# Optimization experiments

Measured on AMD Instinct MI355X. Metric: run time of the kernel, lower is better.

The kernel has to match this reference:

```python
import jax, jax.numpy as jnp
import numpy as np

B, S, T, E, H = 64, 256, 128, 256, 512


def setup_inputs() -> dict:
    key = jax.random.key(0)
    ks = jax.random.split(key, 12)
    sc = 0.05
    return {
        "trg_embed": jax.random.normal(ks[0], (B, T + 1, E), jnp.float32),
        "encoder_hidden": jax.random.normal(ks[1], (B, S, 2 * H), jnp.float32),
        "encoder_final": jax.random.normal(ks[2], (B, H), jnp.float32),
        "src_mask": jnp.ones((B, S), bool),
        "W_ih": jax.random.normal(ks[3], (3 * H, E + 2 * H), jnp.float32) * sc,
        "W_hh": jax.random.normal(ks[4], (3 * H, H), jnp.float32) * sc,
        "b_ih": jnp.zeros((3 * H,), jnp.float32),
        "b_hh": jnp.zeros((3 * H,), jnp.float32),
        "bridge_w": jax.random.normal(ks[5], (H, H), jnp.float32) * sc,
        "bridge_b": jnp.zeros((H,), jnp.float32),
        "key_w": jax.random.normal(ks[6], (H, 2 * H), jnp.float32) * sc,
        "query_w": jax.random.normal(ks[7], (H, H), jnp.float32) * sc,
        "energy_w": jax.random.normal(ks[8], (H,), jnp.float32) * sc,
        "pre_w": jax.random.normal(ks[9], (2 * H, H + 2 * H + E), jnp.float32) * sc,
        "pre_b": jnp.zeros((2 * H,), jnp.float32),
        "max_len": T,
    }


def reference(trg_embed, encoder_hidden, encoder_final, src_mask,
              W_ih, W_hh, b_ih, b_hh, bridge_w, bridge_b,
              key_w, query_w, energy_w, pre_w, pre_b, max_len):
    # bridge: initial decoder state from final encoder state
    h0 = jnp.tanh(encoder_final @ bridge_w.T + bridge_b)          # [B,H]
    # precomputed attention keys
    proj_key = jnp.einsum('bsk,hk->bsh', encoder_hidden, key_w)   # [B,S,H]
    neg = jnp.asarray(-1e9, trg_embed.dtype)

    prev = jnp.swapaxes(trg_embed[:, :max_len], 0, 1)             # [T,B,E]
    curr = jnp.swapaxes(trg_embed[:, 1:max_len + 1], 0, 1)        # [T,B,E] (generate_first)

    def step(h, pc):
        p, c = pc
        # --- additive (Bahdanau) attention, query = current hidden ---
        q = h @ query_w.T                                         # [B,H]
        scores = jnp.tanh(q[:, None, :] + proj_key) @ energy_w    # [B,S]
        scores = jnp.where(src_mask, scores, neg)
        alphas = jax.nn.softmax(scores, axis=-1)                  # [B,S]
        context = jnp.einsum('bs,bsd->bd', alphas, encoder_hidden)  # [B,2H]
        # --- generate_first: pre_output from previous hidden ---
        pre_out = jnp.concatenate([p, h, context], axis=-1) @ pre_w.T + pre_b  # [B,2H]
        # --- GRU cell (torch gate order r, z, n) ---
        x = jnp.concatenate([c, context], axis=-1)                # [B,E+2H]
        gi = x @ W_ih.T + b_ih
        gh = h @ W_hh.T + b_hh
        ir, iz, inn = jnp.split(gi, 3, axis=-1)
        hr, hz, hn = jnp.split(gh, 3, axis=-1)
        r = jax.nn.sigmoid(ir + hr)
        z = jax.nn.sigmoid(iz + hz)
        n = jnp.tanh(inn + r * hn)
        h_new = (1 - z) * n + z * h
        return h_new, (h_new, pre_out, alphas)

    h_fin, (states, pre_outs, attns) = jax.lax.scan(step, h0, (prev, curr))
    return (jnp.swapaxes(states, 0, 1),      # [B,T,H] decoder_states
            h_fin,                            # [B,H] final hidden
            jnp.swapaxes(pre_outs, 0, 1),     # [B,T,2H] pre_output_vectors
            jnp.swapaxes(attns, 0, 1))        # [B,T,S] attention_vectors
```

## Files before the change

### kernel.cpp

```cpp
#include <hip/hip_runtime.h>
#include <hip/hip_fp16.h>

using u32 = unsigned int;

constexpr int B = 64, S = 256, T = 128, E = 256, H = 512, H2 = 1024;
constexpr int TE = (T + 1) * E;

constexpr size_t OUT_HFIN = (size_t)B * T * H;
constexpr size_t OUT_PRE  = OUT_HFIN + (size_t)B * H;
constexpr size_t OUT_ATT  = OUT_PRE + (size_t)B * T * H2;

constexpr size_t WS_HPREV = 0;
constexpr size_t WS_QWT4  = 32768;
constexpr size_t WS_TRGT  = WS_QWT4 + 131072;
constexpr size_t WS_PK2   = WS_TRGT + 1056768;
constexpr size_t WS_HT2R  = WS_PK2 + 4194304;
constexpr size_t WS_QBUF  = WS_HT2R + (size_t)129 * 16384;
constexpr size_t WS_CTXR  = WS_QBUF + (size_t)128 * 16384;
constexpr size_t WS_SEWR  = WS_CTXR + (size_t)128 * 32768;
constexpr size_t WS_BAR   = WS_SEWR + 65536;
constexpr size_t WS_WFR   = WS_BAR + 2048;
constexpr size_t WS_TOTAL = WS_WFR + (size_t)192 * 3584 * 4;

constexpr int L_EHS = 0;
constexpr int L_EWP = 65536;
constexpr int L_HP  = 66688;
constexpr int L_SH2 = 67200;
constexpr int L_UNI = 68224;
constexpr int L_QRED = L_UNI;
constexpr int L_SSE  = L_UNI;
constexpr int L_CRC  = L_UNI;
constexpr int L_SST  = L_UNI + 6144;
constexpr int SMEM_BYTES = L_UNI + 8192;

typedef _Float16 half8 __attribute__((ext_vector_type(8)));
typedef float    f32x4 __attribute__((ext_vector_type(4)));
union UH  { u32 u; _Float16 h[2]; };
union UH8 { uint4 v; half8 h; };

__device__ __forceinline__ u32 pkh(float a, float b) {
  auto v = __builtin_amdgcn_cvt_pkrtz(a, b);
  u32 r; __builtin_memcpy(&r, &v, 4); return r;
}
__device__ __forceinline__ float f16lo(u32 u) { UH x; x.u = u; return (float)x.h[0]; }
__device__ __forceinline__ float f16hi(u32 u) { UH x; x.u = u; return (float)x.h[1]; }

#if __has_builtin(__builtin_amdgcn_fdot2)
__device__ __forceinline__ float fdot2(u32 a, u32 b, float c) {
  typedef _Float16 h2t __attribute__((ext_vector_type(2)));
  h2t av, bv; __builtin_memcpy(&av, &a, 4); __builtin_memcpy(&bv, &b, 4);
  return __builtin_amdgcn_fdot2(av, bv, c, false);
}
#else
__device__ __forceinline__ float fdot2(u32 a, u32 b, float c) {
  return c + f16lo(a) * f16lo(b) + f16hi(a) * f16hi(b);
}
#endif

__device__ __forceinline__ float fast_tanh(float x) {
  return 1.0f - 2.0f / (__expf(2.0f * x) + 1.0f);
}
__device__ __forceinline__ float fast_sigmoid(float x) {
  return 1.0f / (1.0f + __expf(-x));
}
__device__ __forceinline__ float dot4(float4 a, float4 b) {
  return a.x * b.x + a.y * b.y + a.z * b.z + a.w * b.w;
}

__device__ __forceinline__ void st_wt(u32* p, u32 v) {
  __hip_atomic_store(p, v, __ATOMIC_RELAXED, __HIP_MEMORY_SCOPE_AGENT);
}
__device__ __forceinline__ void st_wt_f(float* p, float v) {
  union { float f; u32 u; } c; c.f = v;
  __hip_atomic_store((u32*)p, c.u, __ATOMIC_RELAXED, __HIP_MEMORY_SCOPE_AGENT);
}

__device__ __forceinline__ void gbar_arrive(u32* barg, int p, u32 n) {
  asm volatile("s_waitcnt vmcnt(0) lgkmcnt(0)" ::: "memory");
  __syncthreads();
  if (threadIdx.x == 0) {
    u32 old = __hip_atomic_fetch_add(barg + (p >> 4) * 32, 1u,
                                     __ATOMIC_RELAXED, __HIP_MEMORY_SCOPE_AGENT);
    if ((old & 15u) == 15u) {
      u32 r = __hip_atomic_fetch_add(barg + 768, 1u,
                                     __ATOMIC_RELAXED, __HIP_MEMORY_SCOPE_AGENT);
      if ((r & 15u) == 15u)
        __hip_atomic_store(barg + 800, n, __ATOMIC_RELAXED, __HIP_MEMORY_SCOPE_AGENT);
    }
  }
}
__device__ __forceinline__ void gbar_wait(u32* barg, u32 n) {
  if (threadIdx.x == 0) {
    while (__hip_atomic_load(barg + 800, __ATOMIC_RELAXED,
                             __HIP_MEMORY_SCOPE_AGENT) < n)
      __builtin_amdgcn_s_sleep(2);
  }
  __syncthreads();
  asm volatile("" ::: "memory");
}

__global__ void bridge_kernel(const float* __restrict__ ef,
                              const float* __restrict__ bw,
                              const float* __restrict__ bb,
                              float* __restrict__ h0T) {
  int gid = blockIdx.x * blockDim.x + threadIdx.x;
  int j = gid >> 6, b = gid & 63;
  const float4* w = (const float4*)(bw + (size_t)j * H);
  const float4* e = (const float4*)(ef + (size_t)b * H);
  float acc = 0.f;
#pragma unroll 4
  for (int k = 0; k < H / 4; ++k) acc += dot4(w[k], e[k]);
  h0T[gid] = tanhf(acc + bb[j]);
}

__global__ void packh0_kernel(const float* __restrict__ hprevT, u32* __restrict__ hT2) {
  int idx = blockIdx.x * 512 + threadIdx.x;
  int dp = idx >> 6, b = idx & 63;
  hT2[(size_t)(dp >> 2) * 256 + b * 4 + (dp & 3)] =
      pkh(hprevT[(size_t)(2 * dp) * 64 + b], hprevT[(size_t)(2 * dp + 1) * 64 + b]);
}

__global__ void qwt4_kernel(const float* __restrict__ qw, uint4* __restrict__ qwt4) {
  int kq = blockIdx.x, j = threadIdx.x;
  const float* src = qw + (size_t)j * H + kq * 8;
  uint4 o;
  o.x = pkh(src[0], src[1]); o.y = pkh(src[2], src[3]);
  o.z = pkh(src[4], src[5]); o.w = pkh(src[6], src[7]);
  qwt4[(size_t)kq * 512 + j] = o;
}

__global__ void trgT2_kernel(const float* __restrict__ trg, u32* __restrict__ trgT) {
  int b = blockIdx.x, tid = threadIdx.x;
  for (int i = 0; i < 33; ++i) {
    int idx = i * 512 + tid;
    if (idx >= 129 * 128) break;
    int tt = idx >> 7, kp = idx & 127;
    float2 v = *(const float2*)(trg + (size_t)b * TE + (size_t)tt * 256 + kp * 2);
    trgT[(size_t)tt * 8192 + (size_t)(kp >> 2) * 256 + b * 4 + (kp & 3)] = pkh(v.x, v.y);
  }
}

__global__ void wfrag_kernel(const float* __restrict__ W_ih,
                             const float* __restrict__ W_hh,
                             const float* __restrict__ pre_w,
                             uint4* __restrict__ wfr) {
  const int p = blockIdx.x;
  const bool isGate = p < 128;
  for (int idx = threadIdx.x; idx < 56 * 64; idx += 512) {
    int ks = idx >> 6, lane = idx & 63;
    u32 w4[4];
#pragma unroll
    for (int i = 0; i < 4; ++i) {
      int kp = ks * 16 + (lane >> 4) * 4 + i;
      float a = 0.f, bv = 0.f;
      if (isGate) {
        int row = lane & 15, jo = row >> 2, g = row & 3;
        int j = p * 4 + jo;
        if (kp < 128) {
          if (g < 3) { const float* s_ = W_ih + (size_t)(g * 512 + j) * 1280 + kp * 2; a = s_[0]; bv = s_[1]; }
        } else if (kp < 384) {
          int c = (kp - 128) * 2;
          if (g < 2)       { const float* s_ = W_hh + (size_t)(g * 512 + j) * 512 + c; a = s_[0]; bv = s_[1]; }
          else if (g == 3) { const float* s_ = W_hh + (size_t)(1024 + j) * 512 + c;    a = s_[0]; bv = s_[1]; }
        } else {
          if (g < 3) { const float* s_ = W_ih + (size_t)(g * 512 + j) * 1280 + 256 + (kp - 384) * 2; a = s_[0]; bv = s_[1]; }
        }
      } else {
        int row = (p - 128) * 16 + (lane & 15);
        int c = (kp < 128) ? kp * 2 : (kp < 384) ? 256 + (kp - 128) * 2 : 768 + (kp - 384) * 2;
        const float* s_ = pre_w + (size_t)row * 1792 + c;
        a = s_[0]; bv = s_[1];
      }
      w4[i] = pkh(a, bv);
    }
    wfr[(size_t)p * 3584 + idx] = make_uint4(w4[0], w4[1], w4[2], w4[3]);
  }
}

__global__ void __launch_bounds__(256, 4) projkey2_kernel(
    const float* __restrict__ eh, const float* __restrict__ key_w,
    u32* __restrict__ pk) {
  constexpr int ST = 68;
  __shared__ float ea[64][ST];
  __shared__ float kb[64][ST];
  const int b  = blockIdx.x;
  const int s0 = blockIdx.y * 64;
  const int j0 = blockIdx.z * 64;
  const int tid = threadIdx.x;
  const int rl = tid >> 2, ql = tid & 3;
  const int tx = tid & 15, ty = tid >> 4;
  float acc[4][4] = {};
  const float* esrc = eh + ((size_t)b * S + s0 + rl) * H2;
  const float* ksrc = key_w + (size_t)(j0 + rl) * H2;
  for (int kc = 0; kc < H2; kc += 64) {
    float4 ev[4], kv[4];
#pragma unroll
    for (int m = 0; m < 4; ++m) {
      ev[m] = *(const float4*)(esrc + kc + ql * 16 + m * 4);
      kv[m] = *(const float4*)(ksrc + kc + ql * 16 + m * 4);
    }
    __syncthreads();
#pragma unroll
    for (int m = 0; m < 4; ++m) {
#pragma unroll
      for (int c = 0; c < 4; ++c) {
        int k = ql * 16 + m * 4 + c;
        ea[k][rl] = (&ev[m].x)[c];
        kb[k][rl] = (&kv[m].x)[c];
      }
    }
    __syncthreads();
#pragma unroll 8
    for (int k = 0; k < 64; ++k) {
      float4 a4 = *(const float4*)&ea[k][ty * 4];
      float4 b4 = *(const float4*)&kb[k][tx * 4];
      float av[4] = {a4.x, a4.y, a4.z, a4.w};
      float bv[4] = {b4.x, b4.y, b4.z, b4.w};
#pragma unroll
      for (int i = 0; i < 4; ++i)
#pragma unroll
        for (int jj = 0; jj < 4; ++jj) acc[i][jj] += av[i] * bv[jj];
    }
  }
#pragma unroll
  for (int i = 0; i < 4; ++i) {
    int s = s0 + ty * 4 + i;
    u32 u0 = pkh(acc[i][0], acc[i][1]);
    u32 u1 = pkh(acc[i][2], acc[i][3]);
    *(uint2*)(pk + (size_t)(b * S + s) * 256 + j0 / 2 + tx * 2) = make_uint2(u0, u1);
  }
}

__global__ void __launch_bounds__(512, 4) decoder_loop(
    const float* __restrict__ eh,
    const float* __restrict__ b_ih, const float* __restrict__ b_hh,
    const float* __restrict__ energy_w, const float* __restrict__ pre_b,
    float* __restrict__ out, float* __restrict__ ws) {
  __builtin_amdgcn_fence(__ATOMIC_ACQUIRE, "agent");

  extern __shared__ char smem[];
  u32*   ehs  = (u32*)(smem + L_EHS);
  u32*   ewp  = (u32*)(smem + L_EWP);
  float* shp  = (float*)(smem + L_HP);
  u32*   sh2  = (u32*)(smem + L_SH2);
  float* qred = (float*)(smem + L_QRED);
  float* sse  = (float*)(smem + L_SSE);
  float* crc  = (float*)(smem + L_CRC);
  float* sst  = (float*)(smem + L_SST);

  const uint4* qwt4 = (const uint4*)(ws + WS_QWT4);
  const u32* trgT = (const u32*)(ws + WS_TRGT);
  const u32* pk2  = (const u32*)(ws + WS_PK2);
  const uint4* wfru = (const uint4*)(ws + WS_WFR);
  u32*   ht2r = (u32*)(ws + WS_HT2R);
  u32*   qbr  = (u32*)(ws + WS_QBUF);
  u32*   ctxr = (u32*)(ws + WS_CTXR);
  float* sewr = ws + WS_SEWR;

  const int P = blockIdx.x, tid = threadIdx.x;
  const int g = P >> 8, p = P & 255;
  u32* barg = (u32*)(ws + WS_BAR) + (size_t)g * 1024;
  const int lane = tid & 63, wid = tid >> 6;
  const int b_loc = p >> 3, slice8 = p & 7, s0 = slice8 * 32;
  const int b = g * 32 + b_loc;
  const int bt = wid & 1, kseg = wid >> 1;
  const int bcol = bt * 16 + (lane & 15);
  const int gb = g * 32 + bcol;
  const int g4 = lane >> 4;
  const bool isG = p < 192, isGate = p < 128;

  for (int idx = tid; idx < 32 * 512; idx += 512) {
    int s = idx >> 9, dp = idx & 511;
    float2 v = *(const float2*)(eh + (size_t)(b * 256 + s0 + s) * 1024 + 2 * dp);
    ehs[idx] = pkh(v.x, v.y);
  }
  if (tid < 256)
    ewp[(tid >> 4) * 17 + (tid & 15)] = pkh(energy_w[tid * 2], energy_w[tid * 2 + 1]);
  if (isGate && tid < 128) {
    int jo = tid >> 5, b2 = tid & 31;
    shp[tid] = ws[WS_HPREV + (size_t)(p * 4 + jo) * 64 + (g * 32 + b2)];
  }
  __syncthreads();

  u32 bid = 0;
  for (int t = 0; t < T; ++t) {
    u32* ht2c = ht2r + (size_t)t * 16384;
    u32* ht2n = ht2r + (size_t)(t + 1) * 16384;
    u32* qbt  = qbr + (size_t)t * 16384;
    u32* ctxt = ctxr + (size_t)t * 32768;

    if (tid < 256)
      sh2[tid] = ht2c[(size_t)(tid >> 2) * 256 + b * 4 + (tid & 3)];
    __syncthreads();
    {
      const int jj = slice8 * 64 + lane;
      float acc = 0.f;
#pragma unroll
      for (int kk = 0; kk < 8; ++kk) {
        int kq = wid * 8 + kk;
        uint4 w = qwt4[(size_t)kq * 512 + jj];
        acc = fdot2(w.x, sh2[kq * 4 + 0], acc);
        acc = fdot2(w.y, sh2[kq * 4 + 1], acc);
        acc = fdot2(w.z, sh2[kq * 4 + 2], acc);
        acc = fdot2(w.w, sh2[kq * 4 + 3], acc);
      }
      qred[lane * 9 + wid] = acc;
    }
    __syncthreads();
    if (tid < 32) {
      float q0 = 0.f, q1 = 0.f;
#pragma unroll
      for (int i = 0; i < 8; ++i) { q0 += qred[(2 * tid) * 9 + i]; q1 += qred[(2 * tid + 1) * 9 + i]; }
      st_wt(qbt + (size_t)b * 256 + slice8 * 32 + tid, pkh(q0, q1));
    }
    gbar_arrive(barg, p, ++bid);
    uint4 pk4[4];
    {
      const uint4* pq = (const uint4*)(pk2 + (size_t)(b * 256 + s0 + (tid >> 4)) * 256) + (tid & 15) * 4;
#pragma unroll
      for (int i = 0; i < 4; ++i) pk4[i] = pq[i];
    }
    gbar_wait(barg, bid);

    {
      const int s = tid >> 4, jo = tid & 15;
      const uint4* qrow = (const uint4*)(qbt + (size_t)b * 256) + jo * 4;
      float acc = 0.f;
#pragma unroll
      for (int i = 0; i < 4; ++i) {
        uint4 q4 = qrow[i];
        uint4 pv = pk4[i];
#pragma unroll
        for (int c = 0; c < 4; ++c) {
          u32 qw = (&q4.x)[c];
          u32 w = (&pv.x)[c];
          u32 ew = ewp[jo * 17 + i * 4 + c];
          acc += fast_tanh(f16lo(qw) + f16lo(w)) * f16lo(ew) +
                 fast_tanh(f16hi(qw) + f16hi(w)) * f16hi(ew);
        }
      }
      acc += __shfl_xor(acc, 1); acc += __shfl_xor(acc, 2);
      acc += __shfl_xor(acc, 4); acc += __shfl_xor(acc, 8);
      if ((lane & 15) == 0) {
        float e = __expf(acc);
        out[OUT_ATT + ((size_t)b * T + t) * 256 + s0 + s] = e;
        sse[s] = e;
      }
    }
    __syncthreads();
    if (tid < 32) {
      float sv = sse[tid];
      for (int d = 16; d; d >>= 1) sv += __shfl_xor(sv, d);
      if (tid == 0) st_wt_f(sewr + (size_t)t * 512 + g * 256 + p, sv);
    }
    {
      float a0 = 0.f, a1 = 0.f;
      const u32* er = ehs + tid;
#pragma unroll 8
      for (int s2 = 0; s2 < 32; ++s2) {
        u32 uu = er[s2 * 512];
        float es = sse[s2];
        a0 += es * f16lo(uu);
        a1 += es * f16hi(uu);
      }
      __half2 v2 = __floats2half2_rn(a0, a1);
      unsafeAtomicAdd((__half2*)(ctxt + (size_t)(tid >> 2) * 256 + b * 4 + (tid & 3)), v2);
    }
    gbar_arrive(barg, p, ++bid);
    f32x4 ceh = {0.f, 0.f, 0.f, 0.f}, cct = {0.f, 0.f, 0.f, 0.f};
    if (isG) {
      const u32* embB = trgT + (size_t)(isGate ? t + 1 : t) * 8192;
#pragma unroll
      for (int i = 0; i < 6; ++i) {
        int ks = kseg + 4 * i;
        const u32* bsrc = (ks < 8) ? embB : ht2c;
        int kq = (ks < 8) ? ks : ks - 8;
        UH8 a_, b_;
        a_.v = wfru[((size_t)p * 56 + ks) * 64 + lane];
        b_.v = *(const uint4*)(bsrc + (size_t)((kq * 4 + g4) * 256 + gb * 4));
        ceh = __builtin_amdgcn_mfma_f32_16x16x32_f16(a_.h, b_.h, ceh, 0, 0, 0);
      }
    }
    gbar_wait(barg, bid);

    if (isG) {
#pragma unroll
      for (int i = 6; i < 14; ++i) {
        int ks = kseg + 4 * i;
        UH8 a_, b_;
        a_.v = wfru[((size_t)p * 56 + ks) * 64 + lane];
        b_.v = *(const uint4*)(ctxt + (size_t)(((ks - 24) * 4 + g4) * 256 + gb * 4));
        cct = __builtin_amdgcn_mfma_f32_16x16x32_f16(a_.h, b_.h, cct, 0, 0, 0);
      }
      const float* sp = sewr + (size_t)t * 512 + g * 256 + bcol * 8;
      float4 sv0 = *(const float4*)sp;
      float4 sv1 = *(const float4*)(sp + 4);
      float rv = 1.f / (sv0.x + sv0.y + sv0.z + sv0.w + sv1.x + sv1.y + sv1.z + sv1.w);
      f32x4 tot;
#pragma unroll
      for (int r = 0; r < 4; ++r) tot[r] = ceh[r] + rv * cct[r];
      if (kseg != 0) {
        float* cc = crc + (size_t)((bt * 3 + kseg - 1) * 64 + lane) * 4;
        cc[0] = tot[0]; cc[1] = tot[1]; cc[2] = tot[2]; cc[3] = tot[3];
      }
      __syncthreads();
      if (kseg == 0) {
#pragma unroll
        for (int i = 0; i < 3; ++i) {
          const float* cc = crc + (size_t)((bt * 3 + i) * 64 + lane) * 4;
          tot[0] += cc[0]; tot[1] += cc[1]; tot[2] += cc[2]; tot[3] += cc[3];
        }
        if (isGate) {
          int j = p * 4 + g4;
          float r = fast_sigmoid(tot[0] + b_ih[j] + b_hh[j]);
          float z = fast_sigmoid(tot[1] + b_ih[512 + j] + b_hh[512 + j]);
          float n = fast_tanh((tot[2] + b_ih[1024 + j]) + r * (tot[3] + b_hh[1024 + j]));
          float hp = shp[g4 * 32 + bcol];
          float hv = (1.f - z) * n + z * hp;
          shp[g4 * 32 + bcol] = hv;
          float ho = __shfl_xor(hv, 16);
          if ((g4 & 1) == 0) {
            int jp = p * 2 + (g4 >> 1);
            st_wt(ht2n + (size_t)(jp >> 2) * 256 + gb * 4 + (jp & 3), pkh(hv, ho));
          }
          sst[g4 * 32 + bcol] = hv;
        } else {
          int prow = (p - 128) * 16 + g4 * 4;
          sst[(g4 * 4 + 0) * 32 + bcol] = tot[0] + pre_b[prow + 0];
          sst[(g4 * 4 + 1) * 32 + bcol] = tot[1] + pre_b[prow + 1];
          sst[(g4 * 4 + 2) * 32 + bcol] = tot[2] + pre_b[prow + 2];
          sst[(g4 * 4 + 3) * 32 + bcol] = tot[3] + pre_b[prow + 3];
        }
      }
      __syncthreads();
      if (isGate) {
        if (tid < 32) {
          int b2 = g * 32 + tid;
          float4 o = make_float4(sst[0 * 32 + tid], sst[1 * 32 + tid],
                                 sst[2 * 32 + tid], sst[3 * 32 + tid]);
          *(float4*)(out + ((size_t)b2 * T + t) * 512 + p * 4) = o;
          if (t == T - 1)
            *(float4*)(out + OUT_HFIN + (size_t)b2 * 512 + p * 4) = o;
        }
      } else {
        if (tid < 128) {
          int b2 = g * 32 + (tid & 31), q4 = tid >> 5;
          float4 o = make_float4(sst[(q4 * 4 + 0) * 32 + (tid & 31)],
                                 sst[(q4 * 4 + 1) * 32 + (tid & 31)],
                                 sst[(q4 * 4 + 2) * 32 + (tid & 31)],
                                 sst[(q4 * 4 + 3) * 32 + (tid & 31)]);
          *(float4*)(out + OUT_PRE + ((size_t)b2 * T + t) * 1024 + (p - 128) * 16 + q4 * 4) = o;
        }
      }
    }
    gbar_arrive(barg, p, ++bid);
    if (tid < 32) {
      const float* sp = sewr + (size_t)t * 512 + g * 256 + b_loc * 8;
      float4 sv0 = *(const float4*)sp;
      float4 sv1 = *(const float4*)(sp + 4);
      float rinv = 1.f / (sv0.x + sv0.y + sv0.z + sv0.w + sv1.x + sv1.y + sv1.z + sv1.w);
      out[OUT_ATT + ((size_t)b * T + t) * 256 + s0 + tid] *= rinv;
    }
    if (t == T - 1) break;
    gbar_wait(barg, bid);
  }
}

extern "C" void kernel_launch(void* const* d_in, const int* in_sizes, int n_in,
                              void* d_out, int out_size, void* d_ws, size_t ws_size,
                              hipStream_t stream) {
  const float* trg      = (const float*)d_in[0];
  const float* eh       = (const float*)d_in[1];
  const float* ef       = (const float*)d_in[2];
  const float* W_ih     = (const float*)d_in[4];
  const float* W_hh     = (const float*)d_in[5];
  const float* b_ih     = (const float*)d_in[6];
  const float* b_hh     = (const float*)d_in[7];
  const float* bridge_w = (const float*)d_in[8];
  const float* bridge_b = (const float*)d_in[9];
  const float* key_w    = (const float*)d_in[10];
  const float* query_w  = (const float*)d_in[11];
  const float* energy_w = (const float*)d_in[12];
  const float* pre_w    = (const float*)d_in[13];
  const float* pre_b    = (const float*)d_in[14];
  float* out = (float*)d_out;
  float* ws  = (float*)d_ws;

  hipMemsetAsync((char*)d_ws + WS_CTXR * sizeof(float), 0,
                 (WS_WFR - WS_CTXR) * sizeof(float), stream);
  bridge_kernel<<<64, 512, 0, stream>>>(ef, bridge_w, bridge_b, ws + WS_HPREV);
  packh0_kernel<<<32, 512, 0, stream>>>(ws + WS_HPREV, (u32*)(ws + WS_HT2R));
  qwt4_kernel<<<64, 512, 0, stream>>>(query_w, (uint4*)(ws + WS_QWT4));
  trgT2_kernel<<<64, 512, 0, stream>>>(trg, (u32*)(ws + WS_TRGT));
  wfrag_kernel<<<192, 512, 0, stream>>>(W_ih, W_hh, pre_w, (uint4*)(ws + WS_WFR));
  projkey2_kernel<<<dim3(B, S / 64, H / 64), 256, 0, stream>>>(eh, key_w,
                                                               (u32*)(ws + WS_PK2));

  hipFuncSetAttribute((const void*)decoder_loop,
                      hipFuncAttributeMaxDynamicSharedMemorySize, SMEM_BYTES);
  decoder_loop<<<dim3(512), dim3(512), SMEM_BYTES, stream>>>(
      eh, b_ih, b_hh, energy_w, pre_b, out, ws);
}
```

Measured before the change: 3.580 ms.

## Replace group-wide barrier after query with per-batch 8-block barrier; hoist proj_key loads

The barrier after writing the query vector involved all 256 blocks in a group. It is replaced with a local counter barrier over only the 8 blocks that share a batch row, since only they consume that row's query. The proj_key slice is also loaded once into registers before the time loop rather than reloaded every step. This trades 16 extra VGPRs and a second barrier counter region for fewer global synchronisation round-trips per timestep.

```diff
diff --git a/kernel.cpp b/kernel.cpp
--- a/kernel.cpp
+++ b/kernel.cpp
@@ -19,7 +19,7 @@
 constexpr size_t WS_CTXR  = WS_QBUF + (size_t)128 * 16384;
 constexpr size_t WS_SEWR  = WS_CTXR + (size_t)128 * 32768;
 constexpr size_t WS_BAR   = WS_SEWR + 65536;
-constexpr size_t WS_WFR   = WS_BAR + 2048;
+constexpr size_t WS_WFR   = WS_BAR + 4096;
 constexpr size_t WS_TOTAL = WS_WFR + (size_t)192 * 3584 * 4;
 
 constexpr int L_EHS = 0;
@@ -94,6 +94,18 @@
     while (__hip_atomic_load(barg + 800, __ATOMIC_RELAXED,
                              __HIP_MEMORY_SCOPE_AGENT) < n)
       __builtin_amdgcn_s_sleep(2);
+  }
+  __syncthreads();
+  asm volatile("" ::: "memory");
+}
+
+__device__ __forceinline__ void bbar(u32* cnt, u32 target) {
+  asm volatile("s_waitcnt vmcnt(0) lgkmcnt(0)" ::: "memory");
+  __syncthreads();
+  if (threadIdx.x == 0) {
+    __hip_atomic_fetch_add(cnt, 1u, __ATOMIC_RELAXED, __HIP_MEMORY_SCOPE_AGENT);
+    while (__hip_atomic_load(cnt, __ATOMIC_RELAXED, __HIP_MEMORY_SCOPE_AGENT) < target)
+      __builtin_amdgcn_s_sleep(1);
   }
   __syncthreads();
   asm volatile("" ::: "memory");
@@ -263,6 +275,7 @@
   const int lane = tid & 63, wid = tid >> 6;
   const int b_loc = p >> 3, slice8 = p & 7, s0 = slice8 * 32;
   const int b = g * 32 + b_loc;
+  u32* barb = (u32*)(ws + WS_BAR) + 2048 + (size_t)(g * 32 + b_loc) * 32;
   const int bt = wid & 1, kseg = wid >> 1;
   const int bcol = bt * 16 + (lane & 15);
   const int gb = g * 32 + bcol;
@@ -280,9 +293,17 @@
     int jo = tid >> 5, b2 = tid & 31;
     shp[tid] = ws[WS_HPREV + (size_t)(p * 4 + jo) * 64 + (g * 32 + b2)];
   }
+  u32 pkr[16];
+  {
+    const u32* pq = pk2 + (size_t)(b * 256 + s0 + (tid >> 4)) * 256 + (tid & 15) * 16;
+#pragma unroll
+    for (int i = 0; i < 16; ++i) pkr[i] = pq[i];
+#pragma unroll
+    for (int i = 0; i < 16; ++i) asm volatile("" : "+v"(pkr[i]));
+  }
   __syncthreads();
 
-  u32 bid = 0;
+  u32 gbid = 0;
   for (int t = 0; t < T; ++t) {
     u32* ht2c = ht2r + (size_t)t * 16384;
     u32* ht2n = ht2r + (size_t)(t + 1) * 16384;
@@ -313,14 +334,7 @@
       for (int i = 0; i < 8; ++i) { q0 += qred[(2 * tid) * 9 + i]; q1 += qred[(2 * tid + 1) * 9 + i]; }
       st_wt(qbt + (size_t)b * 256 + slice8 * 32 + tid, pkh(q0, q1));
     }
-    gbar_arrive(barg, p, ++bid);
-    uint4 pk4[4];
-    {
-      const uint4* pq = (const uint4*)(pk2 + (size_t)(b * 256 + s0 + (tid >> 4)) * 256) + (tid & 15) * 4;
-#pragma unroll
-      for (int i = 0; i < 4; ++i) pk4[i] = pq[i];
-    }
-    gbar_wait(barg, bid);
+    bbar(barb, 8u * (u32)(t + 1));
 
     {
       const int s = tid >> 4, jo = tid & 15;
@@ -329,11 +343,10 @@
 #pragma unroll
       for (int i = 0; i < 4; ++i) {
         uint4 q4 = qrow[i];
-        uint4 pv = pk4[i];
 #pragma unroll
         for (int c = 0; c < 4; ++c) {
           u32 qw = (&q4.x)[c];
-          u32 w = (&pv.x)[c];
+          u32 w = pkr[i * 4 + c];
           u32 ew = ewp[jo * 17 + i * 4 + c];
           acc += fast_tanh(f16lo(qw) + f16lo(w)) * f16lo(ew) +
                  fast_tanh(f16hi(qw) + f16hi(w)) * f16hi(ew);
@@ -366,7 +379,7 @@
       __half2 v2 = __floats2half2_rn(a0, a1);
       unsafeAtomicAdd((__half2*)(ctxt + (size_t)(tid >> 2) * 256 + b * 4 + (tid & 3)), v2);
     }
-    gbar_arrive(barg, p, ++bid);
+    gbar_arrive(barg, p, ++gbid);
     f32x4 ceh = {0.f, 0.f, 0.f, 0.f}, cct = {0.f, 0.f, 0.f, 0.f};
     if (isG) {
       const u32* embB = trgT + (size_t)(isGate ? t + 1 : t) * 8192;
@@ -381,7 +394,7 @@
         ceh = __builtin_amdgcn_mfma_f32_16x16x32_f16(a_.h, b_.h, ceh, 0, 0, 0);
       }
     }
-    gbar_wait(barg, bid);
+    gbar_wait(barg, gbid);
 
     if (isG) {
 #pragma unroll
@@ -453,7 +466,7 @@
         }
       }
     }
-    gbar_arrive(barg, p, ++bid);
+    gbar_arrive(barg, p, ++gbid);
     if (tid < 32) {
       const float* sp = sewr + (size_t)t * 512 + g * 256 + b_loc * 8;
       float4 sv0 = *(const float4*)sp;
@@ -462,7 +475,7 @@
       out[OUT_ATT + ((size_t)b * T + t) * 256 + s0 + tid] *= rinv;
     }
     if (t == T - 1) break;
-    gbar_wait(barg, bid);
+    gbar_wait(barg, gbid);
   }
 }
 
```

Result: faster. 3.475 ms (-2.9%).
